# Kernel tuning notes

Measured on AMD Instinct MI355X. Metric: run time of the kernel, lower is better.

Reference implementation:

```python
import jax, jax.numpy as jnp
import numpy as np

NEG_MASK = -10000.0

def setup_inputs() -> dict:
    key = jax.random.key(0)
    k1, k2 = jax.random.split(key)
    T, H, E = 16384, 4096, 64
    hidden_states = jax.random.normal(k1, (T, H), dtype=jnp.float32)
    # router weight [E, H], scaled like typical init so logits are O(1)
    weight = jax.random.normal(k2, (E, H), dtype=jnp.float32) / np.sqrt(H)
    allowed_ids = jnp.arange(32, dtype=jnp.int64 if jax.config.jax_enable_x64 else jnp.int32)
    return {"hidden_states": hidden_states, "weight": weight, "allowed_ids": allowed_ids}

def reference(hidden_states, weight, allowed_ids):
    TOP_K = 8
    E = weight.shape[0]
    # router logits: [T, E]
    router_logits = jnp.einsum("th,eh->te", hidden_states, weight)
    # training-time mask: experts not in allowed_ids get -10000 (allowed_ids are unique,
    # so the scatter of gathered values equals a boolean where-select)
    allowed_mask = jnp.zeros((E,), dtype=bool).at[allowed_ids].set(True)
    router_logits = jnp.where(allowed_mask[None, :], router_logits, NEG_MASK)
    # softmax over experts in float32
    routing_weights = jax.nn.softmax(router_logits.astype(jnp.float32), axis=1)
    # top-k + renorm
    routing_weights, selected_experts = jax.lax.top_k(routing_weights, TOP_K)
    routing_weights = routing_weights / jnp.sum(routing_weights, axis=-1, keepdims=True)
    return (router_logits, routing_weights.astype(hidden_states.dtype), selected_experts)
```

## Files before the change

kernel.cpp:

```cpp
#include <hip/hip_runtime.h>
#include <hip/hip_bf16.h>

typedef __attribute__((ext_vector_type(16))) float f32x16;
typedef __attribute__((ext_vector_type(8))) short short8v;
typedef __attribute__((ext_vector_type(8))) unsigned short ushort8v;

#define T_ROWS 16384
#define H_DIM  4096
#define E_NUM  64
#define TOPK   8
#define MROWS  32
#define KC     128
#define NCH    (H_DIM / KC)
#define WIMG   32768
#define MASK_OFF ((size_t)NCH * WIMG)

__device__ __forceinline__ unsigned short f2bf(float f) {
    unsigned int u = __float_as_uint(f);
    unsigned int r = (u + 0x7fffu + ((u >> 16) & 1u)) >> 16;
    return (unsigned short)r;
}
__device__ __forceinline__ float bf2f(unsigned short h) {
    return __uint_as_float(((unsigned int)h) << 16);
}

__global__ __launch_bounds__(256) void prep_w(
    const float* __restrict__ W, unsigned short* __restrict__ WS,
    const int* __restrict__ ids, int nids)
{
    const int g     = blockIdx.x * 256 + threadIdx.x;
    const int byteo = g * 16;
    const int ch    = byteo >> 15;
    const int rem   = byteo & 32767;
    const int plane = rem >> 14;
    const int rb2   = rem & 16383;
    const int row   = rb2 >> 8;
    const int sb    = rb2 & 255;
    const int bc    = sb ^ ((row & 15) << 4);
    const float* src = W + (size_t)row * H_DIM + ch * KC + (bc >> 1);
    ushort8v o;
#pragma unroll
    for (int j = 0; j < 8; ++j) {
        const float f = src[j];
        const unsigned short hb = f2bf(f);
        o[j] = (plane == 0) ? hb : f2bf(f - bf2f(hb));
    }
    *(ushort8v*)((char*)WS + byteo) = o;

    if (blockIdx.x == 0 && threadIdx.x == 0) {
        unsigned long long mb = 0;
        for (int t = 0; t < nids; ++t) {
            const int e = ids[t];
            if (e >= 0 && e < E_NUM) mb |= (1ull << e);
        }
        *(unsigned long long*)((char*)WS + MASK_OFF) = mb;
    }
}

__global__ __launch_bounds__(512, 2) void router_main(
    const float* __restrict__ X, const unsigned short* __restrict__ WS,
    float* __restrict__ out)
{
    const int tid  = threadIdx.x;
    const int lane = tid & 63;
    const int w    = tid >> 6;
    const int cg   = w & 1;
    const int kh   = w >> 1;
    const int rb   = blockIdx.x * MROWS;
    const int fr32 = lane & 31;
    const int fo   = lane >> 5;

    __shared__ char LDSRAW[49152];
    char* XH = LDSRAW;
    char* XL = LDSRAW + 8192;
    char* WB = LDSRAW + 16384;

    const int srow = tid >> 4;
    const int sc8  = (tid & 15) * 8;
    const float* xg  = X + (size_t)(rb + srow) * H_DIM + sc8;
    const char*  wsg = (const char*)WS;
    const int xbyte = srow * 256 + ((sc8 * 2) ^ ((srow & 15) << 4));

    const int arow = fr32;
    const int brow = cg * 32 + fr32;
    const int asw  = (arow & 15) << 4;
    const int bsw  = (brow & 15) << 4;

    f32x16 acc;
#pragma unroll
    for (int r = 0; r < 16; ++r) acc[r] = 0.f;

    float4 px0 = *(const float4*)(xg);
    float4 px1 = *(const float4*)(xg + 4);
    uint4 pw0 = *(const uint4*)(wsg + 0 * 8192 + tid * 16);
    uint4 pw1 = *(const uint4*)(wsg + 1 * 8192 + tid * 16);
    uint4 pw2 = *(const uint4*)(wsg + 2 * 8192 + tid * 16);
    uint4 pw3 = *(const uint4*)(wsg + 3 * 8192 + tid * 16);

    for (int ch = 0; ch < NCH; ++ch) {
        __syncthreads();
        {
            float v[8] = {px0.x, px0.y, px0.z, px0.w, px1.x, px1.y, px1.z, px1.w};
            ushort8v hv, lv;
#pragma unroll
            for (int j = 0; j < 8; ++j) {
                const unsigned short hb = f2bf(v[j]);
                hv[j] = hb;
                lv[j] = f2bf(v[j] - bf2f(hb));
            }
            *(ushort8v*)(XH + xbyte) = hv;
            *(ushort8v*)(XL + xbyte) = lv;
        }
        *(uint4*)(WB + 0 * 8192 + tid * 16) = pw0;
        *(uint4*)(WB + 1 * 8192 + tid * 16) = pw1;
        *(uint4*)(WB + 2 * 8192 + tid * 16) = pw2;
        *(uint4*)(WB + 3 * 8192 + tid * 16) = pw3;
        __syncthreads();
        if (ch + 1 < NCH) {
            const float* xn = xg + (ch + 1) * KC;
            px0 = *(const float4*)(xn);
            px1 = *(const float4*)(xn + 4);
            const char* wn = wsg + (size_t)(ch + 1) * WIMG;
            pw0 = *(const uint4*)(wn + 0 * 8192 + tid * 16);
            pw1 = *(const uint4*)(wn + 1 * 8192 + tid * 16);
            pw2 = *(const uint4*)(wn + 2 * 8192 + tid * 16);
            pw3 = *(const uint4*)(wn + 3 * 8192 + tid * 16);
        }
#pragma unroll
        for (int ks = 0; ks < 2; ++ks) {
            const int kbyte = kh * 64 + ks * 32 + fo * 16;
            short8v ah = *(const short8v*)(XH + arow * 256 + (kbyte ^ asw));
            short8v al = *(const short8v*)(XL + arow * 256 + (kbyte ^ asw));
            short8v bh = *(const short8v*)(WB + brow * 256 + (kbyte ^ bsw));
            short8v bl = *(const short8v*)(WB + 16384 + brow * 256 + (kbyte ^ bsw));
            acc = __builtin_amdgcn_mfma_f32_32x32x16_bf16(ah, bh, acc, 0, 0, 0);
            acc = __builtin_amdgcn_mfma_f32_32x32x16_bf16(ah, bl, acc, 0, 0, 0);
            acc = __builtin_amdgcn_mfma_f32_32x32x16_bf16(al, bh, acc, 0, 0, 0);
        }
    }

    __syncthreads();
    float* sm = (float*)LDSRAW;
#pragma unroll
    for (int r = 0; r < 16; ++r) {
        const int row = (r & 3) + 8 * (r >> 2) + 4 * fo;
        sm[(kh * 32 + row) * 68 + cg * 32 + fr32] = acc[r];
    }
    __syncthreads();
    if (w >= 2) return;

    const unsigned long long mbits =
        *(const unsigned long long*)((const char*)WS + MASK_OFF);

    const int fr = lane & 15;
    const int fq = lane >> 4;
    float* o_log = out;
    float* o_rw  = out + (size_t)T_ROWS * E_NUM;
    float* o_se  = o_rw + (size_t)T_ROWS * TOPK;

#pragma unroll
    for (int j = 0; j < 4; ++j) {
        const int row_l = w * 16 + fq * 4 + j;
        const int grow  = rb + row_l;
        float a0 = 0.f, a1 = 0.f, a2 = 0.f, a3 = 0.f;
#pragma unroll
        for (int p = 0; p < 4; ++p) {
            a0 += sm[(p * 32 + row_l) * 68 +  0 + fr];
            a1 += sm[(p * 32 + row_l) * 68 + 16 + fr];
            a2 += sm[(p * 32 + row_l) * 68 + 32 + fr];
            a3 += sm[(p * 32 + row_l) * 68 + 48 + fr];
        }
        float mv0 = ((mbits >> ( 0 + fr)) & 1) ? a0 : -10000.0f;
        float mv1 = ((mbits >> (16 + fr)) & 1) ? a1 : -10000.0f;
        float mv2 = ((mbits >> (32 + fr)) & 1) ? a2 : -10000.0f;
        float mv3 = ((mbits >> (48 + fr)) & 1) ? a3 : -10000.0f;
        o_log[(size_t)grow * 64 +  0 + fr] = mv0;
        o_log[(size_t)grow * 64 + 16 + fr] = mv1;
        o_log[(size_t)grow * 64 + 32 + fr] = mv2;
        o_log[(size_t)grow * 64 + 48 + fr] = mv3;

        float m = fmaxf(fmaxf(mv0, mv1), fmaxf(mv2, mv3));
#pragma unroll
        for (int off = 1; off < 16; off <<= 1) m = fmaxf(m, __shfl_xor(m, off));

        float tsum = 0.f, myv = 0.f;
        int   mye  = 0;
#pragma unroll
        for (int t = 0; t < TOPK; ++t) {
            float bv = mv0; int be = fr;
            if (mv1 > bv) { bv = mv1; be = 16 + fr; }
            if (mv2 > bv) { bv = mv2; be = 32 + fr; }
            if (mv3 > bv) { bv = mv3; be = 48 + fr; }
#pragma unroll
            for (int off = 1; off < 16; off <<= 1) {
                float ov = __shfl_xor(bv, off);
                int   oe = __shfl_xor(be, off);
                if (ov > bv || (ov == bv && oe < be)) { bv = ov; be = oe; }
            }
            const float pv = expf(bv - m);
            tsum += pv;
            if (fr == t) { myv = pv; mye = be; }
            if ((be & 15) == fr) {
                const int bn = be >> 4;
                if      (bn == 0) mv0 = -3.4e38f;
                else if (bn == 1) mv1 = -3.4e38f;
                else if (bn == 2) mv2 = -3.4e38f;
                else              mv3 = -3.4e38f;
            }
        }
        if (fr < TOPK) {
            o_rw[(size_t)grow * TOPK + fr] = myv / tsum;
            o_se[(size_t)grow * TOPK + fr] = (float)mye;
        }
    }
}

extern "C" void kernel_launch(void* const* d_in, const int* in_sizes, int n_in,
                              void* d_out, int out_size, void* d_ws, size_t ws_size,
                              hipStream_t stream) {
    const float* X   = (const float*)d_in[0];
    const float* W   = (const float*)d_in[1];
    const int*   ids = (const int*)d_in[2];
    const int    nids = in_sizes[2];
    float* out = (float*)d_out;

    unsigned short* WS = (unsigned short*)d_ws;

    hipLaunchKernelGGL(prep_w, dim3(NCH * WIMG / 16 / 256), dim3(256), 0, stream,
                       W, WS, ids, nids);
    hipLaunchKernelGGL(router_main, dim3(T_ROWS / MROWS), dim3(512), 0, stream,
                       X, WS, out);
}
```

Measured before the change: 93.89 us.

## Pre-pack router weights in MFMA fragment order and load B directly to registers

The weight prep kernel now writes the bf16 hi/lo split of W in per-wave, per-lane MFMA fragment order, so the main kernel loads B operands straight from global memory into registers instead of staging them through LDS. This removes the weight LDS stores and reads and shrinks shared memory from 48KB to 34KB, which allows raising launch bounds to 4 blocks per CU. The chunk loop is unrolled by two with ping-pong register buffers for prefetch. The cost is more global and L2 traffic per wave, since each wave now fetches its own weight fragments, plus higher register pressure under the tighter occupancy bound.

Result: no change. 93.91 us (+0.0%).

```diff
diff --git a/kernel.cpp b/kernel.cpp
--- a/kernel.cpp
+++ b/kernel.cpp
@@ -28,24 +28,24 @@
     const float* __restrict__ W, unsigned short* __restrict__ WS,
     const int* __restrict__ ids, int nids)
 {
-    const int g     = blockIdx.x * 256 + threadIdx.x;
-    const int byteo = g * 16;
-    const int ch    = byteo >> 15;
-    const int rem   = byteo & 32767;
-    const int plane = rem >> 14;
-    const int rb2   = rem & 16383;
-    const int row   = rb2 >> 8;
-    const int sb    = rb2 & 255;
-    const int bc    = sb ^ ((row & 15) << 4);
-    const float* src = W + (size_t)row * H_DIM + ch * KC + (bc >> 1);
+    const int g    = blockIdx.x * 256 + threadIdx.x;
+    const int lane = g & 63;
+    const int j    = (g >> 6) & 3;
+    const int w    = (g >> 8) & 7;
+    const int ch   = g >> 11;
+    const int plane = j & 1;
+    const int ks    = j >> 1;
+    const int row   = (w & 1) * 32 + (lane & 31);
+    const int kk    = ch * KC + (w >> 1) * 32 + ks * 16 + (lane >> 5) * 8;
+    const float* src = W + (size_t)row * H_DIM + kk;
     ushort8v o;
 #pragma unroll
-    for (int j = 0; j < 8; ++j) {
-        const float f = src[j];
+    for (int t = 0; t < 8; ++t) {
+        const float f = src[t];
         const unsigned short hb = f2bf(f);
-        o[j] = (plane == 0) ? hb : f2bf(f - bf2f(hb));
-    }
-    *(ushort8v*)((char*)WS + byteo) = o;
+        o[t] = (plane == 0) ? hb : f2bf(f - bf2f(hb));
+    }
+    *(ushort8v*)((char*)WS + (size_t)g * 16) = o;
 
     if (blockIdx.x == 0 && threadIdx.x == 0) {
         unsigned long long mb = 0;
@@ -57,7 +57,7 @@
     }
 }
 
-__global__ __launch_bounds__(512, 2) void router_main(
+__global__ __launch_bounds__(512, 4) void router_main(
     const float* __restrict__ X, const unsigned short* __restrict__ WS,
     float* __restrict__ out)
 {
@@ -70,21 +70,19 @@
     const int fr32 = lane & 31;
     const int fo   = lane >> 5;
 
-    __shared__ char LDSRAW[49152];
+    __shared__ char LDSRAW[34816];
     char* XH = LDSRAW;
     char* XL = LDSRAW + 8192;
-    char* WB = LDSRAW + 16384;
 
     const int srow = tid >> 4;
     const int sc8  = (tid & 15) * 8;
-    const float* xg  = X + (size_t)(rb + srow) * H_DIM + sc8;
-    const char*  wsg = (const char*)WS;
+    const float* xg = X + (size_t)(rb + srow) * H_DIM + sc8;
     const int xbyte = srow * 256 + ((sc8 * 2) ^ ((srow & 15) << 4));
 
+    const char* wfg = (const char*)WS + (size_t)w * 4096 + (size_t)lane * 16;
+
     const int arow = fr32;
-    const int brow = cg * 32 + fr32;
     const int asw  = (arow & 15) << 4;
-    const int bsw  = (brow & 15) << 4;
 
     f32x16 acc;
 #pragma unroll
@@ -92,52 +90,59 @@
 
     float4 px0 = *(const float4*)(xg);
     float4 px1 = *(const float4*)(xg + 4);
-    uint4 pw0 = *(const uint4*)(wsg + 0 * 8192 + tid * 16);
-    uint4 pw1 = *(const uint4*)(wsg + 1 * 8192 + tid * 16);
-    uint4 pw2 = *(const uint4*)(wsg + 2 * 8192 + tid * 16);
-    uint4 pw3 = *(const uint4*)(wsg + 3 * 8192 + tid * 16);
-
-    for (int ch = 0; ch < NCH; ++ch) {
-        __syncthreads();
-        {
-            float v[8] = {px0.x, px0.y, px0.z, px0.w, px1.x, px1.y, px1.z, px1.w};
-            ushort8v hv, lv;
-#pragma unroll
-            for (int j = 0; j < 8; ++j) {
-                const unsigned short hb = f2bf(v[j]);
-                hv[j] = hb;
-                lv[j] = f2bf(v[j] - bf2f(hb));
-            }
-            *(ushort8v*)(XH + xbyte) = hv;
-            *(ushort8v*)(XL + xbyte) = lv;
-        }
-        *(uint4*)(WB + 0 * 8192 + tid * 16) = pw0;
-        *(uint4*)(WB + 1 * 8192 + tid * 16) = pw1;
-        *(uint4*)(WB + 2 * 8192 + tid * 16) = pw2;
-        *(uint4*)(WB + 3 * 8192 + tid * 16) = pw3;
-        __syncthreads();
-        if (ch + 1 < NCH) {
-            const float* xn = xg + (ch + 1) * KC;
-            px0 = *(const float4*)(xn);
-            px1 = *(const float4*)(xn + 4);
-            const char* wn = wsg + (size_t)(ch + 1) * WIMG;
-            pw0 = *(const uint4*)(wn + 0 * 8192 + tid * 16);
-            pw1 = *(const uint4*)(wn + 1 * 8192 + tid * 16);
-            pw2 = *(const uint4*)(wn + 2 * 8192 + tid * 16);
-            pw3 = *(const uint4*)(wn + 3 * 8192 + tid * 16);
-        }
-#pragma unroll
-        for (int ks = 0; ks < 2; ++ks) {
-            const int kbyte = kh * 64 + ks * 32 + fo * 16;
-            short8v ah = *(const short8v*)(XH + arow * 256 + (kbyte ^ asw));
-            short8v al = *(const short8v*)(XL + arow * 256 + (kbyte ^ asw));
-            short8v bh = *(const short8v*)(WB + brow * 256 + (kbyte ^ bsw));
-            short8v bl = *(const short8v*)(WB + 16384 + brow * 256 + (kbyte ^ bsw));
-            acc = __builtin_amdgcn_mfma_f32_32x32x16_bf16(ah, bh, acc, 0, 0, 0);
-            acc = __builtin_amdgcn_mfma_f32_32x32x16_bf16(ah, bl, acc, 0, 0, 0);
-            acc = __builtin_amdgcn_mfma_f32_32x32x16_bf16(al, bh, acc, 0, 0, 0);
-        }
-    }
+    short8v cA0, cA1, cA2, cA3, cB0, cB1, cB2, cB3;
+    cA0 = *(const short8v*)(wfg);
+    cA1 = *(const short8v*)(wfg + 1024);
+    cA2 = *(const short8v*)(wfg + 2048);
+    cA3 = *(const short8v*)(wfg + 3072);
+
+#define STEP(CH, C0, C1, C2, C3, N0, N1, N2, N3) do {                        \
+        __syncthreads();              \
+        {                                                                    \
+            float v[8] = {px0.x, px0.y, px0.z, px0.w,                        \
+                          px1.x, px1.y, px1.z, px1.w};                       \
+            ushort8v hv, lv;                                                 \
+            _Pragma("unroll")                                                \
+            for (int t = 0; t < 8; ++t) {                                    \
+                const unsigned short hb = f2bf(v[t]);                        \
+                hv[t] = hb;                                                  \
+                lv[t] = f2bf(v[t] - bf2f(hb));                               \
+            }                                                                \
+            *(ushort8v*)(XH + xbyte) = hv;                                   \
+            *(ushort8v*)(XL + xbyte) = lv;                                   \
+        }                                                                    \
+        __syncthreads();                               \
+        if ((CH) + 1 < NCH) {                                                \
+            const float* xn = xg + ((CH) + 1) * KC;                          \
+            px0 = *(const float4*)(xn);                                      \
+            px1 = *(const float4*)(xn + 4);                                  \
+            const char* wi = wfg + (size_t)((CH) + 1) * WIMG;                \
+            N0 = *(const short8v*)(wi);                                      \
+            N1 = *(const short8v*)(wi + 1024);                               \
+            N2 = *(const short8v*)(wi + 2048);                               \
+            N3 = *(const short8v*)(wi + 3072);                               \
+        }                                                                    \
+        {                                                                    \
+            const int kb0 = kh * 64 + fo * 16;                               \
+            short8v ah = *(const short8v*)(XH + arow * 256 + (kb0 ^ asw));   \
+            short8v al = *(const short8v*)(XL + arow * 256 + (kb0 ^ asw));   \
+            acc = __builtin_amdgcn_mfma_f32_32x32x16_bf16(ah, C0, acc, 0, 0, 0); \
+            acc = __builtin_amdgcn_mfma_f32_32x32x16_bf16(ah, C1, acc, 0, 0, 0); \
+            acc = __builtin_amdgcn_mfma_f32_32x32x16_bf16(al, C0, acc, 0, 0, 0); \
+            const int kb1 = kb0 + 32;                                        \
+            short8v ah1 = *(const short8v*)(XH + arow * 256 + (kb1 ^ asw));  \
+            short8v al1 = *(const short8v*)(XL + arow * 256 + (kb1 ^ asw));  \
+            acc = __builtin_amdgcn_mfma_f32_32x32x16_bf16(ah1, C2, acc, 0, 0, 0); \
+            acc = __builtin_amdgcn_mfma_f32_32x32x16_bf16(ah1, C3, acc, 0, 0, 0); \
+            acc = __builtin_amdgcn_mfma_f32_32x32x16_bf16(al1, C2, acc, 0, 0, 0); \
+        }                                                                    \
+    } while (0)
+
+    for (int ch = 0; ch < NCH; ch += 2) {
+        STEP(ch,     cA0, cA1, cA2, cA3, cB0, cB1, cB2, cB3);
+        STEP(ch + 1, cB0, cB1, cB2, cB3, cA0, cA1, cA2, cA3);
+    }
+#undef STEP
 
     __syncthreads();
     float* sm = (float*)LDSRAW;
@@ -226,8 +231,7 @@
 
     unsigned short* WS = (unsigned short*)d_ws;
 
-    hipLaunchKernelGGL(prep_w, dim3(NCH * WIMG / 16 / 256), dim3(256), 0, stream,
-                       W, WS, ids, nids);
+    hipLaunchKernelGGL(prep_w, dim3(256), dim3(256), 0, stream, W, WS, ids, nids);
     hipLaunchKernelGGL(router_main, dim3(T_ROWS / MROWS), dim3(512), 0, stream,
                        X, WS, out);
 }
```

## Double-buffer X/W via direct global-to-LDS loads and drop W low-part split

Applied to the files above, without the earlier changes.

Raises the row tile to 64 and shrinks the K chunk to 64, and loads raw fp32 X and a bf16 W image straight into LDS with global_load_lds into a two-stage double buffer. Waits are now explicit vmcnt waits plus raw barriers. The bf16 hi/lo split of X moves to after the LDS read, next to the MFMA. The W low-part plane is dropped, so each step does two MFMAs instead of three. This cuts register staging, LDS store traffic and MFMA count, but lowers accuracy because W now carries only bf16 precision. Occupancy also changes, since launch_bounds no longer asks for 2 blocks per CU.

After: 105.2 us. 1.12x slower.

```diff
diff --git a/kernel.cpp b/kernel.cpp
--- a/kernel.cpp
+++ b/kernel.cpp
@@ -9,10 +9,10 @@
 #define H_DIM  4096
 #define E_NUM  64
 #define TOPK   8
-#define MROWS  32
-#define KC     128
+#define MROWS  64
+#define KC     64
 #define NCH    (H_DIM / KC)
-#define WIMG   32768
+#define WIMG   8192
 #define MASK_OFF ((size_t)NCH * WIMG)
 
 __device__ __forceinline__ unsigned short f2bf(float f) {
@@ -22,6 +22,11 @@
 }
 __device__ __forceinline__ float bf2f(unsigned short h) {
     return __uint_as_float(((unsigned int)h) << 16);
+}
+__device__ __forceinline__ void gload_lds16(const void* g, void* l) {
+    __builtin_amdgcn_global_load_lds(
+        (const __attribute__((address_space(1))) unsigned int*)g,
+        (__attribute__((address_space(3))) unsigned int*)l, 16, 0, 0);
 }
 
 __global__ __launch_bounds__(256) void prep_w(
@@ -30,21 +35,15 @@
 {
     const int g     = blockIdx.x * 256 + threadIdx.x;
     const int byteo = g * 16;
-    const int ch    = byteo >> 15;
-    const int rem   = byteo & 32767;
-    const int plane = rem >> 14;
-    const int rb2   = rem & 16383;
-    const int row   = rb2 >> 8;
-    const int sb    = rb2 & 255;
-    const int bc    = sb ^ ((row & 15) << 4);
+    const int ch    = byteo >> 13;
+    const int rem   = byteo & 8191;
+    const int row   = rem >> 7;
+    const int sb    = rem & 127;
+    const int bc    = sb ^ ((row & 7) << 4);
     const float* src = W + (size_t)row * H_DIM + ch * KC + (bc >> 1);
     ushort8v o;
 #pragma unroll
-    for (int j = 0; j < 8; ++j) {
-        const float f = src[j];
-        const unsigned short hb = f2bf(f);
-        o[j] = (plane == 0) ? hb : f2bf(f - bf2f(hb));
-    }
+    for (int t = 0; t < 8; ++t) o[t] = f2bf(src[t]);
     *(ushort8v*)((char*)WS + byteo) = o;
 
     if (blockIdx.x == 0 && threadIdx.x == 0) {
@@ -57,86 +56,91 @@
     }
 }
 
-__global__ __launch_bounds__(512, 2) void router_main(
+__global__ __launch_bounds__(512) void router_main(
     const float* __restrict__ X, const unsigned short* __restrict__ WS,
     float* __restrict__ out)
 {
     const int tid  = threadIdx.x;
     const int lane = tid & 63;
     const int w    = tid >> 6;
-    const int cg   = w & 1;
-    const int kh   = w >> 1;
+    const int kh   = w & 1;
+    const int cg   = (w >> 1) & 1;
+    const int rg   = w >> 2;
     const int rb   = blockIdx.x * MROWS;
     const int fr32 = lane & 31;
     const int fo   = lane >> 5;
 
     __shared__ char LDSRAW[49152];
-    char* XH = LDSRAW;
-    char* XL = LDSRAW + 8192;
-    char* WB = LDSRAW + 16384;
-
-    const int srow = tid >> 4;
-    const int sc8  = (tid & 15) * 8;
-    const float* xg  = X + (size_t)(rb + srow) * H_DIM + sc8;
-    const char*  wsg = (const char*)WS;
-    const int xbyte = srow * 256 + ((sc8 * 2) ^ ((srow & 15) << 4));
-
-    const int arow = fr32;
+    char* XF0 = LDSRAW;
+    char* XF1 = LDSRAW + 16384;
+    char* WF0 = LDSRAW + 32768;
+    char* WF1 = LDSRAW + 40960;
+
+    const int xrow0 = w * 8 + (lane >> 4);
+    const int xrow1 = xrow0 + 4;
+    const int xq    = lane & 15;
+    const int xgc0  = xq ^ (xrow0 & 15);
+    const int xgc1  = xq ^ (xrow1 & 15);
+    const float* xs0 = X + (size_t)(rb + xrow0) * H_DIM + xgc0 * 4;
+    const float* xs1 = X + (size_t)(rb + xrow1) * H_DIM + xgc1 * 4;
+    const int xd0 = (w * 2 + 0) * 1024 + lane * 16;
+    const int xd1 = (w * 2 + 1) * 1024 + lane * 16;
+
+    const char* wimg = (const char*)WS;
+    const int   woff = w * 1024 + lane * 16;
+
+    const int arow = rg * 32 + fr32;
+    const int a16  = arow & 15;
     const int brow = cg * 32 + fr32;
-    const int asw  = (arow & 15) << 4;
-    const int bsw  = (brow & 15) << 4;
+    const int bsw  = (brow & 7) << 4;
 
     f32x16 acc;
 #pragma unroll
     for (int r = 0; r < 16; ++r) acc[r] = 0.f;
 
-    float4 px0 = *(const float4*)(xg);
-    float4 px1 = *(const float4*)(xg + 4);
-    uint4 pw0 = *(const uint4*)(wsg + 0 * 8192 + tid * 16);
-    uint4 pw1 = *(const uint4*)(wsg + 1 * 8192 + tid * 16);
-    uint4 pw2 = *(const uint4*)(wsg + 2 * 8192 + tid * 16);
-    uint4 pw3 = *(const uint4*)(wsg + 3 * 8192 + tid * 16);
+    auto stage = [&](int ch, char* xf, char* wf) {
+        gload_lds16(wimg + (size_t)ch * WIMG + woff, wf + woff);
+        gload_lds16(xs0 + ch * KC, xf + xd0);
+        gload_lds16(xs1 + ch * KC, xf + xd1);
+    };
+
+    stage(0, XF0, WF0);
+    stage(1, XF1, WF1);
 
     for (int ch = 0; ch < NCH; ++ch) {
-        __syncthreads();
-        {
-            float v[8] = {px0.x, px0.y, px0.z, px0.w, px1.x, px1.y, px1.z, px1.w};
-            ushort8v hv, lv;
-#pragma unroll
-            for (int j = 0; j < 8; ++j) {
-                const unsigned short hb = f2bf(v[j]);
-                hv[j] = hb;
-                lv[j] = f2bf(v[j] - bf2f(hb));
+        if (ch < NCH - 1) { asm volatile("s_waitcnt vmcnt(3)" ::: "memory"); }
+        else              { asm volatile("s_waitcnt vmcnt(0)" ::: "memory"); }
+        __builtin_amdgcn_sched_barrier(0);
+        __builtin_amdgcn_s_barrier();
+        __builtin_amdgcn_sched_barrier(0);
+
+        const char* xf = (ch & 1) ? XF1 : XF0;
+        const char* wf = (ch & 1) ? WF1 : WF0;
+#pragma unroll
+        for (int ks = 0; ks < 2; ++ks) {
+            const int q0 = kh * 8 + ks * 4 + fo * 2;
+            const float4 a0 = *(const float4*)(xf + arow * 256 + ((q0 ^ a16) << 4));
+            const float4 a1 = *(const float4*)(xf + arow * 256 + (((q0 + 1) ^ a16) << 4));
+            float v[8] = {a0.x, a0.y, a0.z, a0.w, a1.x, a1.y, a1.z, a1.w};
+            short8v ah, al;
+#pragma unroll
+            for (int t = 0; t < 8; ++t) {
+                const unsigned short hb = f2bf(v[t]);
+                ah[t] = (short)hb;
+                al[t] = (short)f2bf(v[t] - bf2f(hb));
             }
-            *(ushort8v*)(XH + xbyte) = hv;
-            *(ushort8v*)(XL + xbyte) = lv;
-        }
-        *(uint4*)(WB + 0 * 8192 + tid * 16) = pw0;
-        *(uint4*)(WB + 1 * 8192 + tid * 16) = pw1;
-        *(uint4*)(WB + 2 * 8192 + tid * 16) = pw2;
-        *(uint4*)(WB + 3 * 8192 + tid * 16) = pw3;
-        __syncthreads();
-        if (ch + 1 < NCH) {
-            const float* xn = xg + (ch + 1) * KC;
-            px0 = *(const float4*)(xn);
-            px1 = *(const float4*)(xn + 4);
-            const char* wn = wsg + (size_t)(ch + 1) * WIMG;
-            pw0 = *(const uint4*)(wn + 0 * 8192 + tid * 16);
-            pw1 = *(const uint4*)(wn + 1 * 8192 + tid * 16);
-            pw2 = *(const uint4*)(wn + 2 * 8192 + tid * 16);
-            pw3 = *(const uint4*)(wn + 3 * 8192 + tid * 16);
-        }
-#pragma unroll
-        for (int ks = 0; ks < 2; ++ks) {
-            const int kbyte = kh * 64 + ks * 32 + fo * 16;
-            short8v ah = *(const short8v*)(XH + arow * 256 + (kbyte ^ asw));
-            short8v al = *(const short8v*)(XL + arow * 256 + (kbyte ^ asw));
-            short8v bh = *(const short8v*)(WB + brow * 256 + (kbyte ^ bsw));
-            short8v bl = *(const short8v*)(WB + 16384 + brow * 256 + (kbyte ^ bsw));
+            const int sb0 = kh * 64 + ks * 32 + fo * 16;
+            short8v bh = *(const short8v*)(wf + brow * 128 + (sb0 ^ bsw));
             acc = __builtin_amdgcn_mfma_f32_32x32x16_bf16(ah, bh, acc, 0, 0, 0);
-            acc = __builtin_amdgcn_mfma_f32_32x32x16_bf16(ah, bl, acc, 0, 0, 0);
             acc = __builtin_amdgcn_mfma_f32_32x32x16_bf16(al, bh, acc, 0, 0, 0);
         }
+
+        asm volatile("s_waitcnt lgkmcnt(0)" ::: "memory");
+        __builtin_amdgcn_sched_barrier(0);
+        __builtin_amdgcn_s_barrier();
+        __builtin_amdgcn_sched_barrier(0);
+        if (ch + 2 < NCH)
+            stage(ch + 2, (ch & 1) ? XF1 : XF0, (ch & 1) ? WF1 : WF0);
     }
 
     __syncthreads();
@@ -144,10 +148,10 @@
 #pragma unroll
     for (int r = 0; r < 16; ++r) {
         const int row = (r & 3) + 8 * (r >> 2) + 4 * fo;
-        sm[(kh * 32 + row) * 68 + cg * 32 + fr32] = acc[r];
+        sm[(kh * 64 + rg * 32 + row) * 68 + cg * 32 + fr32] = acc[r];
     }
     __syncthreads();
-    if (w >= 2) return;
+    if (w >= 4) return;
 
     const unsigned long long mbits =
         *(const unsigned long long*)((const char*)WS + MASK_OFF);
@@ -164,11 +168,11 @@
         const int grow  = rb + row_l;
         float a0 = 0.f, a1 = 0.f, a2 = 0.f, a3 = 0.f;
 #pragma unroll
-        for (int p = 0; p < 4; ++p) {
-            a0 += sm[(p * 32 + row_l) * 68 +  0 + fr];
-            a1 += sm[(p * 32 + row_l) * 68 + 16 + fr];
-            a2 += sm[(p * 32 + row_l) * 68 + 32 + fr];
-            a3 += sm[(p * 32 + row_l) * 68 + 48 + fr];
+        for (int p = 0; p < 2; ++p) {
+            a0 += sm[(p * 64 + row_l) * 68 +  0 + fr];
+            a1 += sm[(p * 64 + row_l) * 68 + 16 + fr];
+            a2 += sm[(p * 64 + row_l) * 68 + 32 + fr];
+            a3 += sm[(p * 64 + row_l) * 68 + 48 + fr];
         }
         float mv0 = ((mbits >> ( 0 + fr)) & 1) ? a0 : -10000.0f;
         float mv1 = ((mbits >> (16 + fr)) & 1) ? a1 : -10000.0f;
@@ -226,8 +230,7 @@
 
     unsigned short* WS = (unsigned short*)d_ws;
 
-    hipLaunchKernelGGL(prep_w, dim3(NCH * WIMG / 16 / 256), dim3(256), 0, stream,
-                       W, WS, ids, nids);
+    hipLaunchKernelGGL(prep_w, dim3(128), dim3(256), 0, stream, W, WS, ids, nids);
     hipLaunchKernelGGL(router_main, dim3(T_ROWS / MROWS), dim3(512), 0, stream,
                        X, WS, out);
 }
```
